# Kernel tuning notes

Hardware: AMD Instinct MI355X
Metric: run time of the kernel (lower is better)

The kernel has to match this reference:

```python
import jax, jax.numpy as jnp
import numpy as np

D_MODEL, EDGE_DIM, HIDDEN = 128, 9, 256
B, N = 2, 512


def setup_inputs() -> dict:
    key = jax.random.key(0)
    ks = jax.random.split(key, 12)
    s = 0.05
    return {
        "z_prime": jax.random.normal(ks[0], (B, N, D_MODEL), jnp.float32),
        "edge_features": jax.random.normal(ks[1], (N, N, EDGE_DIM), jnp.float32),
        "candidate_edge_mask": jax.random.randint(ks[2], (N, N), 0, 2, jnp.int32),
        # organ head params (in, out) layout
        "Wo1": jax.random.normal(ks[3], (D_MODEL, HIDDEN), jnp.float32) * s,
        "bo1": jnp.zeros((HIDDEN,), jnp.float32),
        "Wo2": jax.random.normal(ks[4], (HIDDEN, 1), jnp.float32) * s,
        "bo2": jnp.zeros((1,), jnp.float32),
        # edge head first linear, split by input blocks [zi | zj | edge_feat]
        "We_i": jax.random.normal(ks[5], (D_MODEL, HIDDEN), jnp.float32) * s,
        "We_j": jax.random.normal(ks[6], (D_MODEL, HIDDEN), jnp.float32) * s,
        "We_e": jax.random.normal(ks[7], (EDGE_DIM, HIDDEN), jnp.float32) * s,
        "be1": jnp.zeros((HIDDEN,), jnp.float32),
        "We2": jax.random.normal(ks[8], (HIDDEN, 1), jnp.float32) * s,
        "be2": jnp.zeros((1,), jnp.float32),
    }


def reference(z_prime, edge_features, candidate_edge_mask,
              Wo1, bo1, Wo2, bo2, We_i, We_j, We_e, be1, We2, be2):
    # organ head: sigmoid(MLP(z)) -> (B, N)
    h_o = jax.nn.relu(jnp.einsum('bnd,dh->bnh', z_prime, Wo1) + bo1)
    organ_susceptibility = jax.nn.sigmoid(
        (jnp.einsum('bnh,ho->bno', h_o, Wo2) + bo2).squeeze(-1))

    # edge head: concat([zi, zj, E]) @ W1 decomposed into per-node/per-edge
    # projections (identical math to the concatenated linear).
    pi = jnp.einsum('bnd,dh->bnh', z_prime, We_i)   # (B, N, H) -> broadcast over j
    pj = jnp.einsum('bnd,dh->bnh', z_prime, We_j)   # (B, N, H) -> broadcast over i
    pe = jnp.einsum('ijd,dh->ijh', edge_features, We_e)  # (N, N, H)
    h = jax.nn.relu(pi[:, :, None, :] + pj[:, None, :, :] + pe[None] + be1)
    edge_prob = jax.nn.sigmoid(
        (jnp.einsum('bijh,ho->bijo', h, We2) + be2).squeeze(-1))
    edge_prob = edge_prob * candidate_edge_mask.astype(edge_prob.dtype)[None]
    return (organ_susceptibility, edge_prob)
```

## Files before the change

### kernel.cpp

```cpp
#include <hip/hip_runtime.h>
#include <math.h>
#include <stdint.h>

#define D_MODEL 128
#define EDGE_DIM 9
#define HIDDEN 256
#define BATCH 2
#define NN 512

typedef _Float16 h2v    __attribute__((ext_vector_type(2)));
typedef __fp16   fp16x2 __attribute__((ext_vector_type(2)));
typedef _Float16 f16x8  __attribute__((ext_vector_type(8)));
typedef float    f32x4  __attribute__((ext_vector_type(4)));

struct H8 { h2v v[4]; };

__device__ __forceinline__ uint32_t h2u(h2v v) { return __builtin_bit_cast(uint32_t, v); }
__device__ __forceinline__ h2v u2h(uint32_t u) { return __builtin_bit_cast(h2v, u); }
__device__ __forceinline__ h2v pkrtz(float a, float b) {
    return __builtin_bit_cast(h2v, __builtin_amdgcn_cvt_pkrtz(a, b));
}
__device__ __forceinline__ h2v relu2(h2v v) {
    h2v z = {(_Float16)0.0f, (_Float16)0.0f};
    return __builtin_elementwise_max(v, z);
}
__device__ __forceinline__ float fdot2(h2v a, h2v b, float c) {
    return __builtin_amdgcn_fdot2(__builtin_bit_cast(fp16x2, a),
                                  __builtin_bit_cast(fp16x2, b), c, false);
}
__device__ __forceinline__ float sigmoidf_(float x) { return 1.f / (1.f + expf(-x)); }
__device__ __forceinline__ uint32_t el(const uint4& u, int k) {
    switch (k) { case 0: return u.x; case 1: return u.y; case 2: return u.z; default: return u.w; }
}

__global__ __launch_bounds__(512) void node_mfma_kernel(
    const float* __restrict__ z,
    const float* __restrict__ Wo1,
    const float* __restrict__ bo1,
    const float* __restrict__ Wo2,
    const float* __restrict__ bo2,
    const float* __restrict__ We_i,
    const float* __restrict__ We_j,
    const float* __restrict__ be1,
    float* __restrict__ organ_out,
    uint32_t* __restrict__ pi_h,
    uint32_t* __restrict__ pj_q)
{
    __shared__ uint32_t Wlds[256][68];
    __shared__ float org_part[32][4];

    const int t    = threadIdx.x;
    const int lane = t & 63;
    const int wave = t >> 6;
    const int rb   = blockIdx.x;
    const int m    = blockIdx.y;

    const float* __restrict__ W = (m == 0) ? Wo1 : (m == 1) ? We_i : We_j;

    for (int idx = t; idx < 64 * 256; idx += 512) {
        const int d2 = idx >> 8;
        const int h  = idx & 255;
        const float wlo = W[(2 * d2) * 256 + h];
        const float whi = W[(2 * d2 + 1) * 256 + h];
        Wlds[h][d2 ^ ((h & 7) << 3)] = h2u(pkrtz(wlo, whi));
    }

    const int rt = wave & 1;
    const int cg = wave >> 1;
    const int kg = lane >> 4;
    const int row = rb * 32 + rt * 16 + (lane & 15);

    f16x8 A[4];
#pragma unroll
    for (int kt = 0; kt < 4; ++kt) {
        const float4 za = *(const float4*)&z[(size_t)row * 128 + kt * 32 + kg * 8];
        const float4 zb = *(const float4*)&z[(size_t)row * 128 + kt * 32 + kg * 8 + 4];
        H8 a;
        a.v[0] = pkrtz(za.x, za.y); a.v[1] = pkrtz(za.z, za.w);
        a.v[2] = pkrtz(zb.x, zb.y); a.v[3] = pkrtz(zb.z, zb.w);
        A[kt] = __builtin_bit_cast(f16x8, a);
    }

    __syncthreads();

    f32x4 C[4];
#pragma unroll
    for (int ct = 0; ct < 4; ++ct) {
        const int col = (cg * 4 + ct) * 16 + (lane & 15);
        C[ct] = (f32x4){0.f, 0.f, 0.f, 0.f};
#pragma unroll
        for (int kt = 0; kt < 4; ++kt) {
            const int d2b = (kt * 16 + kg * 4) ^ ((col & 7) << 3);
            const uint4 w = *(const uint4*)&Wlds[col][d2b];
            H8 b;
            b.v[0] = u2h(w.x); b.v[1] = u2h(w.y);
            b.v[2] = u2h(w.z); b.v[3] = u2h(w.w);
            C[ct] = __builtin_amdgcn_mfma_f32_16x16x32_f16(
                        A[kt], __builtin_bit_cast(f16x8, b), C[ct], 0, 0, 0);
        }
    }

    if (m == 0) {
        float s0 = 0.f, s1 = 0.f, s2 = 0.f, s3 = 0.f;
#pragma unroll
        for (int ct = 0; ct < 4; ++ct) {
            const int col = (cg * 4 + ct) * 16 + (lane & 15);
            const float b1 = bo1[col];
            const float w2 = Wo2[col];
            s0 = fmaf(fmaxf(C[ct].x + b1, 0.f), w2, s0);
            s1 = fmaf(fmaxf(C[ct].y + b1, 0.f), w2, s1);
            s2 = fmaf(fmaxf(C[ct].z + b1, 0.f), w2, s2);
            s3 = fmaf(fmaxf(C[ct].w + b1, 0.f), w2, s3);
        }
#pragma unroll
        for (int off = 1; off <= 8; off <<= 1) {
            s0 += __shfl_xor(s0, off, 64);
            s1 += __shfl_xor(s1, off, 64);
            s2 += __shfl_xor(s2, off, 64);
            s3 += __shfl_xor(s3, off, 64);
        }
        if ((lane & 15) == 0) {
            const int rbase = rt * 16 + kg * 4;
            org_part[rbase + 0][cg] = s0;
            org_part[rbase + 1][cg] = s1;
            org_part[rbase + 2][cg] = s2;
            org_part[rbase + 3][cg] = s3;
        }
        __syncthreads();
        if (t < 32) {
            const float s = org_part[t][0] + org_part[t][1]
                          + org_part[t][2] + org_part[t][3] + bo2[0];
            organ_out[rb * 32 + t] = sigmoidf_(s);
        }
    } else if (m == 1) {
#pragma unroll
        for (int ct = 0; ct < 4; ++ct) {
            const int col = (cg * 4 + ct) * 16 + (lane & 15);
            const float bv = be1[col];
            float v0 = C[ct].x + bv, v1 = C[ct].y + bv;
            float v2 = C[ct].z + bv, v3 = C[ct].w + bv;
            const float p0 = __shfl_xor(v0, 1, 64);
            const float p1 = __shfl_xor(v1, 1, 64);
            const float p2 = __shfl_xor(v2, 1, 64);
            const float p3 = __shfl_xor(v3, 1, 64);
            if (!(lane & 1)) {
                const int hp = col >> 1;
                const size_t gr = (size_t)(rb * 32 + rt * 16 + kg * 4);
                pi_h[(gr + 0) * 128 + hp] = h2u(pkrtz(v0, p0));
                pi_h[(gr + 1) * 128 + hp] = h2u(pkrtz(v1, p1));
                pi_h[(gr + 2) * 128 + hp] = h2u(pkrtz(v2, p2));
                pi_h[(gr + 3) * 128 + hp] = h2u(pkrtz(v3, p3));
            }
        }
    } else {
#pragma unroll
        for (int ct = 0; ct < 4; ++ct) {
            const int col = (cg * 4 + ct) * 16 + (lane & 15);
            float v0 = C[ct].x, v1 = C[ct].y, v2 = C[ct].z, v3 = C[ct].w;
            const float p0 = __shfl_xor(v0, 1, 64);
            const float p1 = __shfl_xor(v1, 1, 64);
            const float p2 = __shfl_xor(v2, 1, 64);
            const float p3 = __shfl_xor(v3, 1, 64);
            if (!(lane & 1)) {
                const int hp = col >> 1;
                const size_t gr = (size_t)(rb * 32 + rt * 16 + kg * 4);
                const size_t gbase = (size_t)(hp >> 2) * 1024;
                const int    sub   = hp & 3;
                pj_q[(gbase + gr + 0) * 4 + sub] = h2u(pkrtz(v0, p0));
                pj_q[(gbase + gr + 1) * 4 + sub] = h2u(pkrtz(v1, p1));
                pj_q[(gbase + gr + 2) * 4 + sub] = h2u(pkrtz(v2, p2));
                pj_q[(gbase + gr + 3) * 4 + sub] = h2u(pkrtz(v3, p3));
            }
        }
    }
}

__global__ __launch_bounds__(256) void edge_kernel(
    const float* __restrict__ E,
    const int*   __restrict__ mask,
    const float* __restrict__ We_e,
    const float* __restrict__ We2,
    const float* __restrict__ be2,
    const uint32_t* __restrict__ pi_h,
    const uint32_t* __restrict__ pj_q,
    float* __restrict__ edge_out)
{
    __shared__ __align__(16) uint32_t E_s[8][32][12];
    __shared__ __align__(16) uint32_t wee_s[EDGE_DIM][128];
    __shared__ __align__(16) uint32_t we2_s[128];
    __shared__ __align__(16) uint32_t pi_s[BATCH][8][128];

    const int t    = threadIdx.x;
    const int lane = t & 63;
    const int w    = t >> 6;
    const int bi   = blockIdx.x;
    const int i0   = (bi >> 4) * 8;
    const int j0   = (bi & 15) * 32;

    const int jl = lane & 31;
    const int ih = lane >> 5;
    const int il = 2 * w + ih;

#pragma unroll
    for (int ii = 0; ii < 8; ++ii) {
        const float* src = &E[((size_t)(i0 + ii) * NN + j0) * EDGE_DIM];
        for (int idx = t; idx < 32 * EDGE_DIM; idx += 256) {
            const int jj = idx / 9;
            const int d  = idx - jj * 9;
            const float e = src[idx];
            E_s[ii][jj][d] = h2u(pkrtz(e, e));
        }
    }
    for (int idx = t; idx < EDGE_DIM * 128; idx += 256) {
        const int d  = idx >> 7;
        const int h2 = idx & 127;
        wee_s[d][h2] = h2u(pkrtz(We_e[d * 256 + 2 * h2], We_e[d * 256 + 2 * h2 + 1]));
    }
    if (t < 128) we2_s[t] = h2u(pkrtz(We2[2 * t], We2[2 * t + 1]));
#pragma unroll
    for (int k = 0; k < 2; ++k) {
        const int idx = t + k * 256;
        const int r16 = idx >> 5;
        const int c4  = idx & 31;
        const int b   = r16 >> 3;
        const int ii  = r16 & 7;
        const uint4 v = *(const uint4*)&pi_h[(size_t)(b * NN + i0 + ii) * 128 + c4 * 4];
        *(uint4*)&pi_s[b][ii][c4 * 4] = v;
    }
    __syncthreads();

    h2v e[9];
    {
        const uint32_t* r0 = &E_s[il][jl][0];
        const uint4 a0 = *(const uint4*)(r0);
        const uint4 b0 = *(const uint4*)(r0 + 4);
        e[0]=u2h(a0.x); e[1]=u2h(a0.y); e[2]=u2h(a0.z); e[3]=u2h(a0.w);
        e[4]=u2h(b0.x); e[5]=u2h(b0.y); e[6]=u2h(b0.z); e[7]=u2h(b0.w);
        e[8]=u2h(r0[8]);
    }

    float acc[2] = {0.f, 0.f};

    const uint4* __restrict__ pjQ = (const uint4*)pj_q;
    const int jrow = j0 + jl;

#pragma unroll 1
    for (int hc = 0; hc < 128; hc += 4) {
        uint4 wee4[EDGE_DIM];
#pragma unroll
        for (int d = 0; d < EDGE_DIM; ++d) wee4[d] = *(const uint4*)&wee_s[d][hc];
        const uint4 we24 = *(const uint4*)&we2_s[hc];
        uint4 pi4[2];
        pi4[0] = *(const uint4*)&pi_s[0][il][hc];
        pi4[1] = *(const uint4*)&pi_s[1][il][hc];
        const int g = hc >> 2;
        const uint4 pj40 = pjQ[g * 1024 + jrow];
        const uint4 pj41 = pjQ[g * 1024 + NN + jrow];

#pragma unroll
        for (int k = 0; k < 4; ++k) {
            const h2v w2k = u2h(el(we24, k));
            h2v pe = e[0] * u2h(el(wee4[0], k));
#pragma unroll
            for (int d = 1; d < EDGE_DIM; ++d) pe += e[d] * u2h(el(wee4[d], k));
            h2v t0 = relu2(pe + u2h(el(pj40, k)) + u2h(el(pi4[0], k)));
            acc[0] = fdot2(t0, w2k, acc[0]);
            h2v t1 = relu2(pe + u2h(el(pj41, k)) + u2h(el(pi4[1], k)));
            acc[1] = fdot2(t1, w2k, acc[1]);
        }
    }

    const float b2 = be2[0];
    const int i = i0 + il;
    const float mv = (float)mask[(size_t)i * NN + j0 + jl];
#pragma unroll
    for (int b = 0; b < 2; ++b) {
        const float s = acc[b] + b2;
        edge_out[((size_t)b * NN + i) * NN + j0 + jl] = sigmoidf_(s) * mv;
    }
}

extern "C" void kernel_launch(void* const* d_in, const int* in_sizes, int n_in,
                              void* d_out, int out_size, void* d_ws, size_t ws_size,
                              hipStream_t stream) {
    const float* z    = (const float*)d_in[0];
    const float* E    = (const float*)d_in[1];
    const int*   mask = (const int*)  d_in[2];
    const float* Wo1  = (const float*)d_in[3];
    const float* bo1  = (const float*)d_in[4];
    const float* Wo2  = (const float*)d_in[5];
    const float* bo2  = (const float*)d_in[6];
    const float* We_i = (const float*)d_in[7];
    const float* We_j = (const float*)d_in[8];
    const float* We_e = (const float*)d_in[9];
    const float* be1  = (const float*)d_in[10];
    const float* We2  = (const float*)d_in[11];
    const float* be2  = (const float*)d_in[12];

    float* out_organ = (float*)d_out;
    float* out_edge  = out_organ + BATCH * NN;

    uint32_t* pi_h = (uint32_t*)d_ws;
    uint32_t* pj_q = pi_h + (size_t)BATCH * NN * (HIDDEN/2);

    hipLaunchKernelGGL(node_mfma_kernel,
                       dim3(32, 3), dim3(512), 0, stream,
                       z, Wo1, bo1, Wo2, bo2, We_i, We_j, be1,
                       out_organ, pi_h, pj_q);

    hipLaunchKernelGGL(edge_kernel,
                       dim3(64 * 16), dim3(256), 0, stream,
                       E, mask, We_e, We2, be2, pi_h, pj_q, out_edge);
}
```

Before: 36.89 us.

## Load edge features directly to registers and prefetch pj across iterations

Removes the shared-memory staging of edge features: each thread now reads its own 9 floats from global memory and converts them to half2 in registers, so the stores overlap with the other shared loads before the barrier. The pj loads are also software-pipelined one iteration ahead, with a sched_barrier, to hide global latency inside the hidden-dim loop. Per-thread E reads are strided by 36 bytes and less coalesced than the cooperative staging, and holding the prefetched values raises register pressure.

```diff
diff --git a/kernel.cpp b/kernel.cpp
--- a/kernel.cpp
+++ b/kernel.cpp
@@ -185,7 +185,6 @@
     const uint32_t* __restrict__ pj_q,
     float* __restrict__ edge_out)
 {
-    __shared__ __align__(16) uint32_t E_s[8][32][12];
     __shared__ __align__(16) uint32_t wee_s[EDGE_DIM][128];
     __shared__ __align__(16) uint32_t we2_s[128];
     __shared__ __align__(16) uint32_t pi_s[BATCH][8][128];
@@ -201,16 +200,6 @@
     const int ih = lane >> 5;
     const int il = 2 * w + ih;
 
-#pragma unroll
-    for (int ii = 0; ii < 8; ++ii) {
-        const float* src = &E[((size_t)(i0 + ii) * NN + j0) * EDGE_DIM];
-        for (int idx = t; idx < 32 * EDGE_DIM; idx += 256) {
-            const int jj = idx / 9;
-            const int d  = idx - jj * 9;
-            const float e = src[idx];
-            E_s[ii][jj][d] = h2u(pkrtz(e, e));
-        }
-    }
     for (int idx = t; idx < EDGE_DIM * 128; idx += 256) {
         const int d  = idx >> 7;
         const int h2 = idx & 127;
@@ -227,25 +216,38 @@
         const uint4 v = *(const uint4*)&pi_h[(size_t)(b * NN + i0 + ii) * 128 + c4 * 4];
         *(uint4*)&pi_s[b][ii][c4 * 4] = v;
     }
-    __syncthreads();
 
     h2v e[9];
     {
-        const uint32_t* r0 = &E_s[il][jl][0];
-        const uint4 a0 = *(const uint4*)(r0);
-        const uint4 b0 = *(const uint4*)(r0 + 4);
-        e[0]=u2h(a0.x); e[1]=u2h(a0.y); e[2]=u2h(a0.z); e[3]=u2h(a0.w);
-        e[4]=u2h(b0.x); e[5]=u2h(b0.y); e[6]=u2h(b0.z); e[7]=u2h(b0.w);
-        e[8]=u2h(r0[8]);
-    }
+        const float* eptr = &E[((size_t)(i0 + il) * NN + j0 + jl) * EDGE_DIM];
+        float ef[9];
+#pragma unroll
+        for (int d = 0; d < EDGE_DIM; ++d) ef[d] = eptr[d];
+#pragma unroll
+        for (int d = 0; d < EDGE_DIM; ++d) e[d] = pkrtz(ef[d], ef[d]);
+    }
+
+    __syncthreads();
 
     float acc[2] = {0.f, 0.f};
 
     const uint4* __restrict__ pjQ = (const uint4*)pj_q;
     const int jrow = j0 + jl;
 
+    uint4 pjn0 = pjQ[jrow];
+    uint4 pjn1 = pjQ[NN + jrow];
+
 #pragma unroll 1
     for (int hc = 0; hc < 128; hc += 4) {
+        const int g = hc >> 2;
+        const uint4 pj40 = pjn0;
+        const uint4 pj41 = pjn1;
+        if (g < 31) {
+            pjn0 = pjQ[(g + 1) * 1024 + jrow];
+            pjn1 = pjQ[(g + 1) * 1024 + NN + jrow];
+        }
+        __builtin_amdgcn_sched_barrier(0);
+
         uint4 wee4[EDGE_DIM];
 #pragma unroll
         for (int d = 0; d < EDGE_DIM; ++d) wee4[d] = *(const uint4*)&wee_s[d][hc];
@@ -253,9 +255,6 @@
         uint4 pi4[2];
         pi4[0] = *(const uint4*)&pi_s[0][il][hc];
         pi4[1] = *(const uint4*)&pi_s[1][il][hc];
-        const int g = hc >> 2;
-        const uint4 pj40 = pjQ[g * 1024 + jrow];
-        const uint4 pj41 = pjQ[g * 1024 + NN + jrow];
 
 #pragma unroll
         for (int k = 0; k < 4; ++k) {
```

Measured after the change: 37.55 us. Within noise of the previous version (+1.8%).
